# Kernel optimization log

Hardware: AMD Instinct MI355X
Metric: run time of the kernel (lower is better)

The kernel has to match this reference:

```python
import jax, jax.numpy as jnp
import numpy as np

B, S, H, NH = 2, 2048, 2048, 16
HD = H // NH


def setup_inputs() -> dict:
    key = jax.random.key(0)
    ks = jax.random.split(key, 9)
    s = 1.0 / np.sqrt(H)
    return {
        "hidden_state": jax.random.normal(ks[0], (B, S, H), dtype=jnp.float32),
        "Wq": jax.random.normal(ks[1], (H, H), dtype=jnp.float32) * s,
        "bq": jnp.zeros((H,), dtype=jnp.float32),
        "Wk": jax.random.normal(ks[2], (H, H), dtype=jnp.float32) * s,
        "bk": jnp.zeros((H,), dtype=jnp.float32),
        "Wv": jax.random.normal(ks[3], (H, H), dtype=jnp.float32) * s,
        "bv": jnp.zeros((H,), dtype=jnp.float32),
        "Wo": jax.random.normal(ks[4], (H, H), dtype=jnp.float32) * s,
        "bo": jnp.zeros((H,), dtype=jnp.float32),
    }


def _split_heads(x):
    # [B,S,H] -> [B,NH,S,HD]
    b, s, _ = x.shape
    return x.reshape(b, s, NH, HD).transpose(0, 2, 1, 3)


def reference(hidden_state, Wq, bq, Wk, bk, Wv, bv, Wo, bo):
    q = _split_heads(hidden_state @ Wq.T + bq)
    k = _split_heads(hidden_state @ Wk.T + bk)
    v = _split_heads(hidden_state @ Wv.T + bv)
    scale = 1.0 / jnp.sqrt(jnp.array(HD, dtype=q.dtype))
    scores = jnp.einsum("bhqd,bhkd->bhqk", q, k) * scale
    attn = jax.nn.softmax(scores, axis=-1)
    out = jnp.einsum("bhqk,bhkd->bhqd", attn, v)  # [B,NH,S,HD]
    out = out.transpose(0, 2, 1, 3).reshape(hidden_state.shape[0], -1, H)
    return out @ Wo.T + bo
```

## Files before the change

kernel.cpp:

```cpp
#include <hip/hip_runtime.h>
#include <hip/hip_bf16.h>
#include <stdint.h>

#define B_ 2
#define S_ 2048
#define H_ 2048
#define NH_ 16
#define HD_ 128
#define M_ (B_*S_)

typedef __attribute__((ext_vector_type(8))) short short8_t;
typedef __attribute__((ext_vector_type(4))) float floatx4;

__device__ __forceinline__ short f2bf(float f) {
  union { float f; uint32_t u; } x; x.f = f;
  const uint32_t u = x.u;
  return (short)((u + 0x7FFFu + ((u >> 16) & 1u)) >> 16);
}

__device__ __forceinline__ void gload_lds16(const void* g, void* l) {
  __builtin_amdgcn_global_load_lds(
      (const __attribute__((address_space(1))) void*)g,
      (__attribute__((address_space(3))) void*)l, 16, 0, 0);
}

__global__ __launch_bounds__(256)
void cast_all(const float* __restrict__ h,  const float* __restrict__ wq,
              const float* __restrict__ wk, const float* __restrict__ wv,
              const float* __restrict__ wo,
              short* __restrict__ hB,  short* __restrict__ wqB,
              short* __restrict__ wkB, short* __restrict__ wvB,
              short* __restrict__ woB) {
  const int blk = blockIdx.x;
  const float* src; short* dst; int off;
  if      (blk <  4096) { src = h;  dst = hB;  off = blk; }
  else if (blk <  6144) { src = wq; dst = wqB; off = blk - 4096; }
  else if (blk <  8192) { src = wk; dst = wkB; off = blk - 6144; }
  else if (blk < 10240) { src = wv; dst = wvB; off = blk - 8192; }
  else                  { src = wo; dst = woB; off = blk - 10240; }
  const int i = (off * 256 + threadIdx.x) * 8;
  typedef __attribute__((ext_vector_type(4))) float f4;
  const f4 a = *(const f4*)(src + i);
  const f4 b = *(const f4*)(src + i + 4);
  short8_t o;
  o[0] = f2bf(a[0]); o[1] = f2bf(a[1]); o[2] = f2bf(a[2]); o[3] = f2bf(a[3]);
  o[4] = f2bf(b[0]); o[5] = f2bf(b[1]); o[6] = f2bf(b[2]); o[7] = f2bf(b[3]);
  *(short8_t*)(dst + i) = o;
}

template<int MT, int MODE>
__device__ __forceinline__
void gemm_body(const short* __restrict__ A, const short* __restrict__ Bm,
               const float* __restrict__ bias, void* __restrict__ C,
               const int m0, const int n0, const int N, const int K) {
  constexpr int MI = MT / 32;
  __shared__ short As[MT * 64];
  __shared__ short Bs[128 * 64];
  const int tid = threadIdx.x;
  const int wv = tid >> 6, ln = tid & 63;
  const int lr = ln >> 4, lc = ln & 15;
  const int wm = (wv >> 1) * (MT / 2);
  const int wn = (wv & 1) * 64;
  const int srow = ln >> 3;
  const int sc   = (ln & 7) ^ srow;

  floatx4 acc[MI][4] = {};
  const short* aP[MT / 32];
  const short* bP[4];
#pragma unroll
  for (int i = 0; i < MT / 32; ++i)
    aP[i] = A + (size_t)(m0 + wv * (MT / 4) + i * 8 + srow) * K + sc * 8;
#pragma unroll
  for (int i = 0; i < 4; ++i)
    bP[i] = Bm + (size_t)(n0 + wv * 32 + i * 8 + srow) * K + sc * 8;
  const int sw = (lc & 7) << 3;

  for (int k0 = 0; k0 < K; k0 += 64) {
#pragma unroll
    for (int i = 0; i < MT / 32; ++i)
      gload_lds16(aP[i] + k0, &As[(wv * (MT / 4) + i * 8) * 64]);
#pragma unroll
    for (int i = 0; i < 4; ++i)
      gload_lds16(bP[i] + k0, &Bs[(wv * 32 + i * 8) * 64]);
    __syncthreads();
#pragma unroll
    for (int ksq = 0; ksq < 2; ++ksq) {
      short8_t af[MI], bf[4];
#pragma unroll
      for (int t = 0; t < MI; ++t)
        af[t] = *(const short8_t*)&As[(wm + t * 16 + lc) * 64 + ((ksq * 32 + lr * 8) ^ sw)];
#pragma unroll
      for (int t = 0; t < 4; ++t)
        bf[t] = *(const short8_t*)&Bs[(wn + t * 16 + lc) * 64 + ((ksq * 32 + lr * 8) ^ sw)];
#pragma unroll
      for (int i = 0; i < MI; ++i)
#pragma unroll
        for (int j = 0; j < 4; ++j)
          acc[i][j] = __builtin_amdgcn_mfma_f32_16x16x32_bf16(af[i], bf[j], acc[i][j], 0, 0, 0);
    }
    __syncthreads();
  }

#pragma unroll
  for (int i = 0; i < MI; ++i) {
#pragma unroll
    for (int j = 0; j < 4; ++j) {
      const int col = n0 + wn + j * 16 + lc;
      const float bv = bias[col];
#pragma unroll
      for (int r = 0; r < 4; ++r) {
        const int row = m0 + wm + i * 16 + lr * 4 + r;
        const float v = acc[i][j][r] + bv;
        if (MODE == 1) ((float*)C)[(size_t)row * N + col] = v;
        else           ((short*)C)[(size_t)row * N + col] = f2bf(v);
      }
    }
  }
}

__global__ __launch_bounds__(256)
void gemm_qkv(const short* __restrict__ A,
              const short* __restrict__ W0, const short* __restrict__ W1, const short* __restrict__ W2,
              const float* __restrict__ b0, const float* __restrict__ b1, const float* __restrict__ b2,
              short* __restrict__ C0, short* __restrict__ C1, short* __restrict__ C2) {
  const int sel = blockIdx.x >> 4;
  const short* Bm   = sel == 0 ? W0 : (sel == 1 ? W1 : W2);
  const float* bias = sel == 0 ? b0 : (sel == 1 ? b1 : b2);
  short* C          = sel == 0 ? C0 : (sel == 1 ? C1 : C2);
  gemm_body<128, 0>(A, Bm, bias, C, blockIdx.y * 128, (blockIdx.x & 15) * 128, H_, H_);
}

__global__ __launch_bounds__(256)
void gemm_out(const short* __restrict__ A, const short* __restrict__ Bm,
              const float* __restrict__ bias, float* __restrict__ C) {
  gemm_body<64, 1>(A, Bm, bias, C, blockIdx.y * 64, blockIdx.x * 128, H_, H_);
}

__global__ __launch_bounds__(256)
void arrange_v(const short* __restrict__ V, short* __restrict__ Vt) {
  __shared__ short T[64][72];
  const int b = blockIdx.z;
  const int s0 = blockIdx.x * 64, c0 = blockIdx.y * 64;
  const int t = threadIdx.x;
  const int r = t >> 3, c8 = (t & 7) * 8;
  const int kt = s0 >> 6;
#pragma unroll
  for (int p = 0; p < 2; ++p) {
    const int row = p * 32 + r;
    *(short8_t*)&T[row][c8] =
        *(const short8_t*)&V[(size_t)(b * S_ + s0 + row) * H_ + c0 + c8];
  }
  __syncthreads();
#pragma unroll
  for (int p = 0; p < 2; ++p) {
    const int row = p * 32 + r;
    const int gcol = c0 + row;
    const int hh = gcol >> 7, d = gcol & 127;
    short8_t o;
#pragma unroll
    for (int j = 0; j < 8; ++j) o[j] = T[c8 + j][row];
    const int chunk = (c8 >> 3) ^ (d & 7);
    *(short8_t*)&Vt[((((size_t)(b * 16 + hh) * 32 + kt) * 128 + d) << 6) + chunk * 8] = o;
  }
}

__global__ __launch_bounds__(512, 4)
void attention(const short* __restrict__ Q, const short* __restrict__ Kg,
               const short* __restrict__ Vt, short* __restrict__ O) {
  __shared__ short Ks[64 * 128];
  __shared__ short Vs[128 * 64];
  __shared__ short Ps[128 * 64];

  const int tid = threadIdx.x;
  const int wv = tid >> 6, ln = tid & 63;
  const int lr = ln >> 4, lc = ln & 15;
  const int bh = blockIdx.y, b = bh >> 4, h = bh & 15;
  const int qw = blockIdx.x * 128 + wv * 16;

  const short* Qp  = Q  + ((size_t)(b * S_ + qw)) * H_ + h * HD_;
  const short* VtB = Vt + (size_t)bh * (S_ * HD_);

  const int kl0 = ln >> 4,        c0_ = (ln & 15) ^ (kl0 & 7);
  const int kl1 = 4 + (ln >> 4),  c1_ = (ln & 15) ^ (kl1 & 7);
  const short* kp0 = Kg + ((size_t)(b * S_ + wv * 8 + kl0) * H_ + h * HD_ + c0_ * 8);
  const short* kp1 = Kg + ((size_t)(b * S_ + wv * 8 + kl1) * H_ + h * HD_ + c1_ * 8);

  short8_t qf[4];
#pragma unroll
  for (int ksq = 0; ksq < 4; ++ksq)
    qf[ksq] = *(const short8_t*)&Qp[(size_t)lc * H_ + ksq * 32 + lr * 8];

  floatx4 oacc[8] = {};
  float lsum[4] = {};
  const float csc = 0.08838834764831845f * 1.4426950408889634f;
  const int sA = (lc & 7) << 3;
  const int i0 = wv * 1024 + ln * 8;

  for (int kt = 0; kt < S_ / 64; ++kt) {
    const size_t kadv = (size_t)kt * 64 * H_;
    const size_t tb = (size_t)kt * 8192;
    gload_lds16(kp0 + kadv,          &Ks[(wv * 8) * 128]);
    gload_lds16(kp1 + kadv,          &Ks[(wv * 8 + 4) * 128]);
    gload_lds16(VtB + tb + i0,       &Vs[wv * 1024]);
    gload_lds16(VtB + tb + i0 + 512, &Vs[wv * 1024 + 512]);
    __syncthreads();

    floatx4 sacc[4] = {};
#pragma unroll
    for (int ksq = 0; ksq < 4; ++ksq) {
#pragma unroll
      for (int tj = 0; tj < 4; ++tj) {
        const short8_t kf =
            *(const short8_t*)&Ks[(tj * 16 + lc) * 128 + ((ksq * 32 + lr * 8) ^ sA)];
        sacc[tj] = __builtin_amdgcn_mfma_f32_16x16x32_bf16(qf[ksq], kf, sacc[tj], 0, 0, 0);
      }
    }

#pragma unroll
    for (int tj = 0; tj < 4; ++tj) {
#pragma unroll
      for (int r = 0; r < 4; ++r) {
        const float p = exp2f(sacc[tj][r] * csc);
        const uint32_t u = __float_as_uint(p);
        const int row = wv * 16 + lr * 4 + r;
        Ps[row * 64 + ((tj * 16 + lc) ^ ((row & 7) << 3))] = (short)(u >> 16);
        lsum[r] += __uint_as_float(u & 0xffff0000u);
      }
    }

#pragma unroll
    for (int ks = 0; ks < 2; ++ks) {
      const short8_t pf =
          *(const short8_t*)&Ps[(wv * 16 + lc) * 64 + ((ks * 32 + lr * 8) ^ sA)];
#pragma unroll
      for (int tj = 0; tj < 8; ++tj) {
        const short8_t vf =
            *(const short8_t*)&Vs[(tj * 16 + lc) * 64 + ((ks * 32 + lr * 8) ^ sA)];
        oacc[tj] = __builtin_amdgcn_mfma_f32_16x16x32_bf16(pf, vf, oacc[tj], 0, 0, 0);
      }
    }
    __syncthreads();
  }

  float inv[4];
#pragma unroll
  for (int r = 0; r < 4; ++r) {
    float l = lsum[r];
    l += __shfl_xor(l, 1);
    l += __shfl_xor(l, 2);
    l += __shfl_xor(l, 4);
    l += __shfl_xor(l, 8);
    inv[r] = 1.0f / l;
  }
  __syncthreads();
  short* Kw = &Ks[wv * 1024];
  short* Op = O + ((size_t)(b * S_ + qw)) * H_ + h * HD_;
  const int orow = ln >> 2, ocp = (ln & 3) * 2;
#pragma unroll
  for (int hh = 0; hh < 2; ++hh) {
#pragma unroll
    for (int tj = 0; tj < 4; ++tj)
#pragma unroll
      for (int r = 0; r < 4; ++r) {
        const int row = lr * 4 + r;
        Kw[row * 64 + ((tj * 16 + lc) ^ ((row & 7) << 3))] =
            f2bf(oacc[hh * 4 + tj][r] * inv[r]);
      }
    const short8_t v0 = *(const short8_t*)&Kw[orow * 64 + ((ocp * 8) ^ ((orow & 7) << 3))];
    const short8_t v1 = *(const short8_t*)&Kw[orow * 64 + (((ocp + 1) * 8) ^ ((orow & 7) << 3))];
    *(short8_t*)&Op[(size_t)orow * H_ + hh * 64 + ocp * 8]     = v0;
    *(short8_t*)&Op[(size_t)orow * H_ + hh * 64 + ocp * 8 + 8] = v1;
  }
}

extern "C" void kernel_launch(void* const* d_in, const int* in_sizes, int n_in,
                              void* d_out, int out_size, void* d_ws, size_t ws_size,
                              hipStream_t stream) {
  const float* hidden = (const float*)d_in[0];
  const float* Wq = (const float*)d_in[1];
  const float* bq = (const float*)d_in[2];
  const float* Wk = (const float*)d_in[3];
  const float* bk = (const float*)d_in[4];
  const float* Wv = (const float*)d_in[5];
  const float* bv = (const float*)d_in[6];
  const float* Wo = (const float*)d_in[7];
  const float* bo = (const float*)d_in[8];
  float* out = (float*)d_out;

  char* ws = (char*)d_ws;
  short* hB  = (short*)(ws);
  short* WqB = (short*)(ws + (16u << 20));
  short* WkB = (short*)(ws + (24u << 20));
  short* WvB = (short*)(ws + (32u << 20));
  short* WoB = (short*)(ws + (40u << 20));
  short* Qb  = (short*)(ws + (48u << 20));
  short* Kb  = (short*)(ws + (64u << 20));
  short* Vb  = (short*)(ws + (80u << 20));
  short* Vtb = (short*)(ws + (96u << 20));
  short* Ob  = (short*)(ws + (112u << 20));

  cast_all<<<12288, 256, 0, stream>>>(hidden, Wq, Wk, Wv, Wo, hB, WqB, WkB, WvB, WoB);

  gemm_qkv<<<dim3(48, M_ / 128), 256, 0, stream>>>(hB, WqB, WkB, WvB, bq, bk, bv, Qb, Kb, Vb);

  arrange_v<<<dim3(S_ / 64, H_ / 64, B_), 256, 0, stream>>>(Vb, Vtb);

  attention<<<dim3(S_ / 128, B_ * NH_), 512, 0, stream>>>(Qb, Kb, Vtb, Ob);

  gemm_out<<<dim3(H_ / 128, M_ / 64), 256, 0, stream>>>(Ob, WoB, bo, out);
}
```

Before: 424.3 us.

## Switch attention to 32x32x16 MFMA with 4 waves, enlarge output GEMM tile

The attention kernel is rebuilt around 32x32x16 bf16 MFMA instructions. Each of 4 waves now handles 32 query rows instead of 8 waves handling 16, so every K/V fragment loaded from LDS feeds more math. The output is written straight to global memory instead of being staged through LDS. Separately, the output projection GEMM moves from 64-row to 128-row tiles, which halves the block count. The costs are higher register pressure (16-float accumulators, 16 partial sums), fewer blocks in flight, and output stores that are not fully coalesced.

```diff
diff --git a/kernel.cpp b/kernel.cpp
--- a/kernel.cpp
+++ b/kernel.cpp
@@ -11,6 +11,7 @@
 
 typedef __attribute__((ext_vector_type(8))) short short8_t;
 typedef __attribute__((ext_vector_type(4))) float floatx4;
+typedef __attribute__((ext_vector_type(16))) float floatx16;
 
 __device__ __forceinline__ short f2bf(float f) {
   union { float f; uint32_t u; } x; x.f = f;
@@ -48,28 +49,26 @@
   *(short8_t*)(dst + i) = o;
 }
 
-template<int MT, int MODE>
+template<int MODE>
 __device__ __forceinline__
 void gemm_body(const short* __restrict__ A, const short* __restrict__ Bm,
                const float* __restrict__ bias, void* __restrict__ C,
                const int m0, const int n0, const int N, const int K) {
-  constexpr int MI = MT / 32;
-  __shared__ short As[MT * 64];
+  __shared__ short As[128 * 64];
   __shared__ short Bs[128 * 64];
   const int tid = threadIdx.x;
   const int wv = tid >> 6, ln = tid & 63;
   const int lr = ln >> 4, lc = ln & 15;
-  const int wm = (wv >> 1) * (MT / 2);
-  const int wn = (wv & 1) * 64;
+  const int wm = (wv >> 1) * 64, wn = (wv & 1) * 64;
   const int srow = ln >> 3;
   const int sc   = (ln & 7) ^ srow;
 
-  floatx4 acc[MI][4] = {};
-  const short* aP[MT / 32];
+  floatx4 acc[4][4] = {};
+  const short* aP[4];
   const short* bP[4];
 #pragma unroll
-  for (int i = 0; i < MT / 32; ++i)
-    aP[i] = A + (size_t)(m0 + wv * (MT / 4) + i * 8 + srow) * K + sc * 8;
+  for (int i = 0; i < 4; ++i)
+    aP[i] = A + (size_t)(m0 + wv * 32 + i * 8 + srow) * K + sc * 8;
 #pragma unroll
   for (int i = 0; i < 4; ++i)
     bP[i] = Bm + (size_t)(n0 + wv * 32 + i * 8 + srow) * K + sc * 8;
@@ -77,23 +76,23 @@
 
   for (int k0 = 0; k0 < K; k0 += 64) {
 #pragma unroll
-    for (int i = 0; i < MT / 32; ++i)
-      gload_lds16(aP[i] + k0, &As[(wv * (MT / 4) + i * 8) * 64]);
+    for (int i = 0; i < 4; ++i)
+      gload_lds16(aP[i] + k0, &As[(wv * 32 + i * 8) * 64]);
 #pragma unroll
     for (int i = 0; i < 4; ++i)
       gload_lds16(bP[i] + k0, &Bs[(wv * 32 + i * 8) * 64]);
     __syncthreads();
 #pragma unroll
     for (int ksq = 0; ksq < 2; ++ksq) {
-      short8_t af[MI], bf[4];
-#pragma unroll
-      for (int t = 0; t < MI; ++t)
+      short8_t af[4], bf[4];
+#pragma unroll
+      for (int t = 0; t < 4; ++t)
         af[t] = *(const short8_t*)&As[(wm + t * 16 + lc) * 64 + ((ksq * 32 + lr * 8) ^ sw)];
 #pragma unroll
       for (int t = 0; t < 4; ++t)
         bf[t] = *(const short8_t*)&Bs[(wn + t * 16 + lc) * 64 + ((ksq * 32 + lr * 8) ^ sw)];
 #pragma unroll
-      for (int i = 0; i < MI; ++i)
+      for (int i = 0; i < 4; ++i)
 #pragma unroll
         for (int j = 0; j < 4; ++j)
           acc[i][j] = __builtin_amdgcn_mfma_f32_16x16x32_bf16(af[i], bf[j], acc[i][j], 0, 0, 0);
@@ -102,7 +101,7 @@
   }
 
 #pragma unroll
-  for (int i = 0; i < MI; ++i) {
+  for (int i = 0; i < 4; ++i) {
 #pragma unroll
     for (int j = 0; j < 4; ++j) {
       const int col = n0 + wn + j * 16 + lc;
@@ -127,13 +126,13 @@
   const short* Bm   = sel == 0 ? W0 : (sel == 1 ? W1 : W2);
   const float* bias = sel == 0 ? b0 : (sel == 1 ? b1 : b2);
   short* C          = sel == 0 ? C0 : (sel == 1 ? C1 : C2);
-  gemm_body<128, 0>(A, Bm, bias, C, blockIdx.y * 128, (blockIdx.x & 15) * 128, H_, H_);
+  gemm_body<0>(A, Bm, bias, C, blockIdx.y * 128, (blockIdx.x & 15) * 128, H_, H_);
 }
 
 __global__ __launch_bounds__(256)
 void gemm_out(const short* __restrict__ A, const short* __restrict__ Bm,
               const float* __restrict__ bias, float* __restrict__ C) {
-  gemm_body<64, 1>(A, Bm, bias, C, blockIdx.y * 64, blockIdx.x * 128, H_, H_);
+  gemm_body<1>(A, Bm, bias, C, blockIdx.y * 128, blockIdx.x * 128, H_, H_);
 }
 
 __global__ __launch_bounds__(256)
@@ -164,7 +163,7 @@
   }
 }
 
-__global__ __launch_bounds__(512, 4)
+__global__ __launch_bounds__(256, 2)
 void attention(const short* __restrict__ Q, const short* __restrict__ Kg,
                const short* __restrict__ Vt, short* __restrict__ O) {
   __shared__ short Ks[64 * 128];
@@ -173,104 +172,102 @@
 
   const int tid = threadIdx.x;
   const int wv = tid >> 6, ln = tid & 63;
-  const int lr = ln >> 4, lc = ln & 15;
+  const int l32 = ln & 31, lh = ln >> 5;
   const int bh = blockIdx.y, b = bh >> 4, h = bh & 15;
-  const int qw = blockIdx.x * 128 + wv * 16;
+  const int qw = blockIdx.x * 128 + wv * 32;
 
   const short* Qp  = Q  + ((size_t)(b * S_ + qw)) * H_ + h * HD_;
-  const short* VtB = Vt + (size_t)bh * (S_ * HD_);
-
-  const int kl0 = ln >> 4,        c0_ = (ln & 15) ^ (kl0 & 7);
-  const int kl1 = 4 + (ln >> 4),  c1_ = (ln & 15) ^ (kl1 & 7);
-  const short* kp0 = Kg + ((size_t)(b * S_ + wv * 8 + kl0) * H_ + h * HD_ + c0_ * 8);
-  const short* kp1 = Kg + ((size_t)(b * S_ + wv * 8 + kl1) * H_ + h * HD_ + c1_ * 8);
-
-  short8_t qf[4];
-#pragma unroll
-  for (int ksq = 0; ksq < 4; ++ksq)
-    qf[ksq] = *(const short8_t*)&Qp[(size_t)lc * H_ + ksq * 32 + lr * 8];
-
-  floatx4 oacc[8] = {};
-  float lsum[4] = {};
+  const short* VtB = Vt + (size_t)bh * (S_ * HD_) + (size_t)wv * 2048 + ln * 8;
+
+  const short* kp[4];
+#pragma unroll
+  for (int j = 0; j < 4; ++j) {
+    const int key = wv * 16 + j * 4 + (ln >> 4);
+    const int sc = (ln & 15) ^ (key & 7);
+    kp[j] = Kg + (size_t)(b * S_ + key) * H_ + h * HD_ + sc * 8;
+  }
+
+  short8_t qf[8];
+#pragma unroll
+  for (int ksq = 0; ksq < 8; ++ksq)
+    qf[ksq] = *(const short8_t*)&Qp[(size_t)l32 * H_ + ksq * 16 + lh * 8];
+
+  floatx16 oacc[4] = {};
+  float lsum[16] = {};
   const float csc = 0.08838834764831845f * 1.4426950408889634f;
-  const int sA = (lc & 7) << 3;
-  const int i0 = wv * 1024 + ln * 8;
 
   for (int kt = 0; kt < S_ / 64; ++kt) {
     const size_t kadv = (size_t)kt * 64 * H_;
-    const size_t tb = (size_t)kt * 8192;
-    gload_lds16(kp0 + kadv,          &Ks[(wv * 8) * 128]);
-    gload_lds16(kp1 + kadv,          &Ks[(wv * 8 + 4) * 128]);
-    gload_lds16(VtB + tb + i0,       &Vs[wv * 1024]);
-    gload_lds16(VtB + tb + i0 + 512, &Vs[wv * 1024 + 512]);
+#pragma unroll
+    for (int j = 0; j < 4; ++j)
+      gload_lds16(kp[j] + kadv, &Ks[(wv * 16 + j * 4) * 128]);
+#pragma unroll
+    for (int j = 0; j < 4; ++j)
+      gload_lds16(VtB + (size_t)kt * 8192 + j * 512, &Vs[wv * 2048 + j * 512]);
     __syncthreads();
 
-    floatx4 sacc[4] = {};
-#pragma unroll
-    for (int ksq = 0; ksq < 4; ++ksq) {
-#pragma unroll
-      for (int tj = 0; tj < 4; ++tj) {
+    floatx16 sacc[2] = {};
+#pragma unroll
+    for (int kh = 0; kh < 2; ++kh) {
+      const int key = kh * 32 + l32;
+      const int swk = (key & 7) * 8;
+#pragma unroll
+      for (int ksq = 0; ksq < 8; ++ksq) {
         const short8_t kf =
-            *(const short8_t*)&Ks[(tj * 16 + lc) * 128 + ((ksq * 32 + lr * 8) ^ sA)];
-        sacc[tj] = __builtin_amdgcn_mfma_f32_16x16x32_bf16(qf[ksq], kf, sacc[tj], 0, 0, 0);
+            *(const short8_t*)&Ks[key * 128 + (((ksq * 2 + lh) * 8) ^ swk)];
+        sacc[kh] = __builtin_amdgcn_mfma_f32_32x32x16_bf16(qf[ksq], kf, sacc[kh], 0, 0, 0);
       }
     }
 
 #pragma unroll
-    for (int tj = 0; tj < 4; ++tj) {
-#pragma unroll
-      for (int r = 0; r < 4; ++r) {
-        const float p = exp2f(sacc[tj][r] * csc);
+    for (int kh = 0; kh < 2; ++kh) {
+#pragma unroll
+      for (int r = 0; r < 16; ++r) {
+        const float p = exp2f(sacc[kh][r] * csc);
         const uint32_t u = __float_as_uint(p);
-        const int row = wv * 16 + lr * 4 + r;
-        Ps[row * 64 + ((tj * 16 + lc) ^ ((row & 7) << 3))] = (short)(u >> 16);
+        const int row = wv * 32 + (r & 3) + 8 * (r >> 2) + 4 * lh;
+        const int col = kh * 32 + l32;
+        Ps[row * 64 + ((((col >> 3) ^ (row & 7)) * 8) | (col & 7))] = (short)(u >> 16);
         lsum[r] += __uint_as_float(u & 0xffff0000u);
       }
     }
 
-#pragma unroll
-    for (int ks = 0; ks < 2; ++ks) {
+    const int prow = wv * 32 + l32;
+    const int swp = (prow & 7) * 8;
+#pragma unroll
+    for (int kf = 0; kf < 4; ++kf) {
       const short8_t pf =
-          *(const short8_t*)&Ps[(wv * 16 + lc) * 64 + ((ks * 32 + lr * 8) ^ sA)];
-#pragma unroll
-      for (int tj = 0; tj < 8; ++tj) {
+          *(const short8_t*)&Ps[prow * 64 + (((kf * 2 + lh) * 8) ^ swp)];
+#pragma unroll
+      for (int dt = 0; dt < 4; ++dt) {
+        const int d = dt * 32 + l32;
         const short8_t vf =
-            *(const short8_t*)&Vs[(tj * 16 + lc) * 64 + ((ks * 32 + lr * 8) ^ sA)];
-        oacc[tj] = __builtin_amdgcn_mfma_f32_16x16x32_bf16(pf, vf, oacc[tj], 0, 0, 0);
+            *(const short8_t*)&Vs[d * 64 + (((kf * 2 + lh) * 8) ^ ((d & 7) * 8))];
+        oacc[dt] = __builtin_amdgcn_mfma_f32_32x32x16_bf16(pf, vf, oacc[dt], 0, 0, 0);
       }
     }
     __syncthreads();
   }
 
-  float inv[4];
-#pragma unroll
-  for (int r = 0; r < 4; ++r) {
+  float inv[16];
+#pragma unroll
+  for (int r = 0; r < 16; ++r) {
     float l = lsum[r];
     l += __shfl_xor(l, 1);
     l += __shfl_xor(l, 2);
     l += __shfl_xor(l, 4);
     l += __shfl_xor(l, 8);
+    l += __shfl_xor(l, 16);
     inv[r] = 1.0f / l;
   }
-  __syncthreads();
-  short* Kw = &Ks[wv * 1024];
   short* Op = O + ((size_t)(b * S_ + qw)) * H_ + h * HD_;
-  const int orow = ln >> 2, ocp = (ln & 3) * 2;
-#pragma unroll
-  for (int hh = 0; hh < 2; ++hh) {
-#pragma unroll
-    for (int tj = 0; tj < 4; ++tj)
-#pragma unroll
-      for (int r = 0; r < 4; ++r) {
-        const int row = lr * 4 + r;
-        Kw[row * 64 + ((tj * 16 + lc) ^ ((row & 7) << 3))] =
-            f2bf(oacc[hh * 4 + tj][r] * inv[r]);
-      }
-    const short8_t v0 = *(const short8_t*)&Kw[orow * 64 + ((ocp * 8) ^ ((orow & 7) << 3))];
-    const short8_t v1 = *(const short8_t*)&Kw[orow * 64 + (((ocp + 1) * 8) ^ ((orow & 7) << 3))];
-    *(short8_t*)&Op[(size_t)orow * H_ + hh * 64 + ocp * 8]     = v0;
-    *(short8_t*)&Op[(size_t)orow * H_ + hh * 64 + ocp * 8 + 8] = v1;
-  }
+#pragma unroll
+  for (int dt = 0; dt < 4; ++dt)
+#pragma unroll
+    for (int r = 0; r < 16; ++r) {
+      const int rowl = (r & 3) + 8 * (r >> 2) + 4 * lh;
+      Op[(size_t)rowl * H_ + dt * 32 + l32] = f2bf(oacc[dt][r] * inv[r]);
+    }
 }
 
 extern "C" void kernel_launch(void* const* d_in, const int* in_sizes, int n_in,
@@ -305,7 +302,7 @@
 
   arrange_v<<<dim3(S_ / 64, H_ / 64, B_), 256, 0, stream>>>(Vb, Vtb);
 
-  attention<<<dim3(S_ / 128, B_ * NH_), 512, 0, stream>>>(Qb, Kb, Vtb, Ob);
-
-  gemm_out<<<dim3(H_ / 128, M_ / 64), 256, 0, stream>>>(Ob, WoB, bo, out);
-}
+  attention<<<dim3(S_ / 128, B_ * NH_), 256, 0, stream>>>(Qb, Kb, Vtb, Ob);
+
+  gemm_out<<<dim3(H_ / 128, M_ / 128), 256, 0, stream>>>(Ob, WoB, bo, out);
+}
```

After: 395.4 us. 1.07x faster.
